# Kernel tuning notes

Hardware: AMD Instinct MI355X
Metric: run time of the kernel (lower is better)

## Reference

```python
import jax, jax.numpy as jnp
import numpy as np
from jax import lax

D = 256; NH = 8; LYR = 2; G = 64; K = G * G; T = 4; EC = 32
B = 4; N = 512; CITY = 256; DFF = 4 * D

def _conv(x, w):
    return lax.conv_general_dilated(x, w, (1, 1), 'SAME', dimension_numbers=('NCHW', 'OIHW', 'NCHW'))

def _ln(x, w, b):
    m = x.mean(-1, keepdims=True)
    v = ((x - m) ** 2).mean(-1, keepdims=True)
    return (x - m) / jnp.sqrt(v + 1e-5) * w + b

def _mlp(x, w1, b1, w2, b2):
    return jax.nn.gelu(x @ w1 + b1) @ w2 + b2

def setup_inputs():
    key = jax.random.key(0)
    ks = iter(jax.random.split(key, 64))
    def nrm(shape, s=0.02):
        return jax.random.normal(next(ks), shape, jnp.float32) * s
    return {
        'meas_xy': jax.random.uniform(next(ks), (B, N, 2), jnp.float32),
        'meas_v': jax.random.normal(next(ks), (B, N), jnp.float32),
        'bs_xy': jax.random.uniform(next(ks), (B, 1, 2), jnp.float32),
        'task_id': jax.random.randint(next(ks), (B,), 0, T),
        'city': jax.random.uniform(next(ks), (B, CITY, CITY), jnp.float32),
        'mp_w1': nrm((3, D)), 'mp_b1': jnp.zeros((D,)), 'mp_w2': nrm((D, D)), 'mp_b2': jnp.zeros((D,)),
        'bp_w1': nrm((2, D)), 'bp_b1': jnp.zeros((D,)), 'bp_w2': nrm((D, D)), 'bp_b2': jnp.zeros((D,)),
        'env_w1': nrm((EC, 1, 3, 3)), 'env_b1': jnp.zeros((EC,)),
        'env_w2': nrm((EC, EC, 3, 3)), 'env_b2': jnp.zeros((EC,)),
        'env_w3': nrm((D, EC, 1, 1)), 'env_b3': jnp.zeros((D,)),
        'task_emb': nrm((T, D)), 'tp_w': nrm((D, D)), 'tp_b': jnp.zeros((D,)),
        'grid_pos': nrm((K, D)),
        'blk_dens_w': nrm((LYR, D)), 'blk_dens_b': jnp.zeros((LYR, D)),
        'blk_ln1_w': jnp.ones((LYR, D)), 'blk_ln1_b': jnp.zeros((LYR, D)),
        'blk_wq': nrm((LYR, D, D)), 'blk_bq': jnp.zeros((LYR, D)),
        'blk_wk': nrm((LYR, D, D)), 'blk_bk': jnp.zeros((LYR, D)),
        'blk_wv': nrm((LYR, D, D)), 'blk_bv': jnp.zeros((LYR, D)),
        'blk_wo': nrm((LYR, D, D)), 'blk_bo': jnp.zeros((LYR, D)),
        'blk_ln2_w': jnp.ones((LYR, D)), 'blk_ln2_b': jnp.zeros((LYR, D)),
        'blk_ff_w1': nrm((LYR, D, DFF)), 'blk_ff_b1': jnp.zeros((LYR, DFF)),
        'blk_ff_w2': nrm((LYR, DFF, D)), 'blk_ff_b2': jnp.zeros((LYR, D)),
        'tfp_w': nrm((T, D, D)), 'tfp_b': jnp.zeros((T, D)),
        'head_w': nrm((D, 1)), 'head_b': jnp.zeros((1,)),
    }

def reference(meas_xy, meas_v, bs_xy, task_id, city, mp_w1, mp_b1, mp_w2, mp_b2, bp_w1, bp_b1, bp_w2, bp_b2, env_w1, env_b1, env_w2, env_b2, env_w3, env_b3, task_emb, tp_w, tp_b, grid_pos, blk_dens_w, blk_dens_b, blk_ln1_w, blk_ln1_b, blk_wq, blk_bq, blk_wk, blk_bk, blk_wv, blk_bv, blk_wo, blk_bo, blk_ln2_w, blk_ln2_b, blk_ff_w1, blk_ff_b1, blk_ff_w2, blk_ff_b2, tfp_w, tfp_b, head_w, head_b):
    b = meas_xy.shape[0]
    dh = D // NH
    # normalized grid cell centers, [K,2] in (x,y) order
    c = (jnp.arange(G, dtype=jnp.float32) + 0.5) / G
    gy, gx = jnp.meshgrid(c, c, indexing='ij')
    grid_xy = jnp.stack([gx, gy], -1).reshape(K, 2)
    meas_tok = _mlp(jnp.concatenate([meas_xy, meas_v[..., None]], -1), mp_w1, mp_b1, mp_w2, mp_b2)
    bs_tok = _mlp(bs_xy, bp_w1, bp_b1, bp_w2, bp_b2)
    src = jnp.concatenate([meas_tok, bs_tok], 1)       # [B,Ns,D]
    src_xy = jnp.concatenate([meas_xy, bs_xy], 1)      # [B,Ns,2]
    # distance bias: [B,K,Ns]
    attn_bias = -jnp.linalg.norm(grid_xy[None, :, None, :] - src_xy[:, None, :, :], axis=-1)
    # gaussian measurement density: [B,K]
    diff = grid_xy[None, :, None, :] - meas_xy[:, None, :, :]
    dist2 = (diff * diff).sum(-1)
    sigma = 0.08
    density = jnp.exp(-dist2 / (2.0 * sigma * sigma)).mean(-1)
    # env branch: nearest-resize city to GxG, small CNN
    idx = jnp.floor(jnp.arange(G) * (city.shape[1] / G)).astype(jnp.int32)
    city_grid = city[:, idx][:, :, idx][:, None]       # [B,1,G,G]
    h = jax.nn.gelu(_conv(city_grid, env_w1) + env_b1[None, :, None, None])
    h = jax.nn.gelu(_conv(h, env_w2) + env_b2[None, :, None, None])
    env_map = _conv(h, env_w3) + env_b3[None, :, None, None]
    env_grid = env_map.transpose(0, 2, 3, 1).reshape(b, K, D)
    task_vec = (task_emb[task_id] @ tp_w + tp_b)[:, None, :]
    grid = grid_pos[None] + task_vec + env_grid
    inv_sqrt = jnp.float32(1.0 / np.sqrt(dh))
    for l in range(LYR):
        # density modulation injected into the grid latent
        g = grid + density[..., None] * blk_dens_w[l] + blk_dens_b[l]
        hn = _ln(g, blk_ln1_w[l], blk_ln1_b[l])
        q = (hn @ blk_wq[l] + blk_bq[l]).reshape(b, K, NH, dh)
        kk = (src @ blk_wk[l] + blk_bk[l]).reshape(b, -1, NH, dh)
        vv = (src @ blk_wv[l] + blk_bv[l]).reshape(b, -1, NH, dh)
        scores = jnp.einsum('bkhd,bnhd->bhkn', q, kk) * inv_sqrt + attn_bias[:, None]
        a = jax.nn.softmax(scores, -1)
        o = jnp.einsum('bhkn,bnhd->bkhd', a, vv).reshape(b, K, D) @ blk_wo[l] + blk_bo[l]
        g = g + o
        g = g + _mlp(_ln(g, blk_ln2_w[l], blk_ln2_b[l]), blk_ff_w1[l], blk_ff_b1[l], blk_ff_w2[l], blk_ff_b2[l])
        grid = g
    # per-sample task projection from the weight bank
    tf = jax.nn.gelu(jnp.einsum('bkd,bdh->bkh', grid, tfp_w[task_id]) + tfp_b[task_id][:, None, :])
    logits = (tf @ head_w + head_b)[..., 0].reshape(b, G, G)
    return logits
```

## Files before the change

### kernel.cpp

```cpp
#include <hip/hip_runtime.h>
#include <hip/hip_bf16.h>
#include <math.h>

#define D 256
#define NH 8
#define DH 32
#define LYR 2
#define G 64
#define KK 4096
#define T 4
#define EC 32
#define B 4
#define N 512
#define CITY 256
#define DFF 1024
#define NS 513
#define NSP 544
#define MSRC 2052
#define MSRCP 2176
#define ISQ 0.17677669529663687f
#define LOG2E 1.4426950408889634f

typedef short bf16x8 __attribute__((ext_vector_type(8)));
typedef float f32x4 __attribute__((ext_vector_type(4)));

__device__ __forceinline__ float gelu_f(float x) {
    const float c2 = 2.f * 0.7978845608028654f * LOG2E;
    float u = x + 0.044715f * x * x * x;
    float e = __builtin_amdgcn_exp2f(-c2 * u);
    return x * __builtin_amdgcn_rcpf(1.f + e);
}

__device__ __forceinline__ unsigned short f2bf(float f) {
    unsigned int u = __float_as_uint(f);
    unsigned int r = (u + 0x7FFFu + ((u >> 16) & 1u)) >> 16;
    return (unsigned short)r;
}

__device__ __forceinline__ float bf2f(unsigned short u) {
    return __uint_as_float((unsigned)u << 16);
}

__device__ __forceinline__ unsigned cvtpk(float a, float b) {
    unsigned r;
    asm("v_cvt_pk_bf16_f32 %0, %1, %2" : "=v"(r) : "v"(a), "v"(b));
    return r;
}

__device__ __forceinline__ void gl2lds16(const unsigned short* g, unsigned short* l) {
    __builtin_amdgcn_global_load_lds(
        (const __attribute__((address_space(1))) unsigned int*)g,
        (__attribute__((address_space(3))) unsigned int*)l, 16, 0, 0);
}

__global__ __launch_bounds__(256) void pre1_k(
    const float* __restrict__ wq, const float* __restrict__ wk,
    const float* __restrict__ wv, const float* __restrict__ wo,
    const float* __restrict__ ff1, const float* __restrict__ ff2,
    const float* __restrict__ tfp,
    const float* __restrict__ bk, const float* __restrict__ bv,
    unsigned short* __restrict__ wqT, unsigned short* __restrict__ kvT,
    unsigned short* __restrict__ woT, unsigned short* __restrict__ ff1T,
    unsigned short* __restrict__ ff2T, unsigned short* __restrict__ tfpT,
    float* __restrict__ kvbias,
    const float* __restrict__ meas_xy, const float* __restrict__ meas_v,
    const float* __restrict__ bs_xy,
    const float* __restrict__ mp_w1, const float* __restrict__ mp_b1,
    const float* __restrict__ mp_w2, const float* __restrict__ mp_b2,
    const float* __restrict__ bp_w1, const float* __restrict__ bp_b1,
    const float* __restrict__ bp_w2, const float* __restrict__ bp_b2,
    unsigned short* __restrict__ srcbf, float* __restrict__ src_xy,
    float* __restrict__ dens,
    const float* __restrict__ city, const float* __restrict__ env_w1,
    const float* __restrict__ env_b1, float* __restrict__ h1,
    const float* __restrict__ task_emb, const int* __restrict__ task_id,
    const float* __restrict__ tp_w, const float* __restrict__ tp_b,
    float* __restrict__ tvec,
    unsigned short* __restrict__ khd, unsigned short* __restrict__ vch)
{
    __shared__ float sh[1088];
    int bx = blockIdx.x;
    int tid = threadIdx.x;
    if (bx < 1792) {
        const float* src; unsigned short* dst;
        int Kd, Nn, nmat, rowOff = 0, t; size_t matStride;
        if (bx < 512) {
            int job = bx >> 7; t = bx & 127;
            Kd = 256; Nn = 256; nmat = 2;
            if (job == 0)      { src = wq; dst = wqT; matStride = 65536; }
            else if (job == 1) { src = wk; dst = kvT; matStride = 131072; }
            else if (job == 2) { src = wv; dst = kvT; matStride = 131072; rowOff = 256; }
            else               { src = wo; dst = woT; matStride = 65536; }
            if ((t & 63) == 0 && job == 1) kvbias[(t >> 6) * 512 + tid] = bk[(t >> 6) * 256 + tid];
            if ((t & 63) == 0 && job == 2) kvbias[(t >> 6) * 512 + 256 + tid] = bv[(t >> 6) * 256 + tid];
        } else if (bx < 1024) { t = bx - 512;  src = ff1; dst = ff1T; Kd = 256;  Nn = 1024; nmat = 2; matStride = 262144; }
        else if (bx < 1536)   { t = bx - 1024; src = ff2; dst = ff2T; Kd = 1024; Nn = 256;  nmat = 2; matStride = 262144; }
        else                  { t = bx - 1536; src = tfp; dst = tfpT; Kd = 256;  Nn = 256;  nmat = 4; matStride = 65536; }
        int tn = Nn / 32, perMat = tn * (Kd / 32);
        int mat = t / perMat;
        int rem = t - mat * perMat;
        int nb = (rem % tn) * 32, kb = (rem / tn) * 32;
        const float* s = src + (size_t)mat * Kd * Nn;
        unsigned short* d = dst + (size_t)mat * matStride;
        float (*tb)[33] = (float (*)[33])sh;
        int tx = tid & 31, ty = tid >> 5;
        #pragma unroll
        for (int i = 0; i < 4; i++)
            tb[ty + i * 8][tx] = s[(size_t)(kb + ty + i * 8) * Nn + nb + tx];
        __syncthreads();
        #pragma unroll
        for (int i = 0; i < 4; i++)
            d[(size_t)(rowOff + nb + ty + i * 8) * Kd + kb + tx] = f2bf(tb[tx][ty + i * 8]);
    } else if (bx < 3968) {
        int id = bx - 1792;
        int dd = tid;
        if (id >= B * N + B) {
            srcbf[(size_t)id * D + dd] = 0;
            return;
        }
        float* hid = sh;
        int row;
        const float *w1, *b1, *w2, *b2;
        float x0, x1, x2 = 0.f;
        int nin;
        if (id < B * N) {
            int b = id >> 9, n = id & 511;
            x0 = meas_xy[(b * N + n) * 2 + 0];
            x1 = meas_xy[(b * N + n) * 2 + 1];
            x2 = meas_v[b * N + n];
            w1 = mp_w1; b1 = mp_b1; w2 = mp_w2; b2 = mp_b2; nin = 3;
            row = b * NS + n;
        } else {
            int b = id - B * N;
            x0 = bs_xy[b * 2 + 0];
            x1 = bs_xy[b * 2 + 1];
            w1 = bp_w1; b1 = bp_b1; w2 = bp_w2; b2 = bp_b2; nin = 2;
            row = b * NS + N;
        }
        float h = x0 * w1[dd] + x1 * w1[D + dd] + b1[dd];
        if (nin == 3) h += x2 * w1[2 * D + dd];
        hid[dd] = gelu_f(h);
        __syncthreads();
        float o = b2[dd];
        for (int j = 0; j < D; j++) o += hid[j] * w2[j * D + dd];
        srcbf[(size_t)row * D + dd] = f2bf(o);
        if (dd == 0) { src_xy[row * 2 + 0] = x0; src_xy[row * 2 + 1] = x1; }
    } else if (bx < 4032) {
        int blk = bx - 3968;
        int b = blk >> 4, kc = blk & 15;
        int k = kc * 256 + tid;
        float* mx = sh; float* my = sh + 512;
        for (int i = tid; i < N; i += 256) {
            mx[i] = meas_xy[(b * N + i) * 2 + 0];
            my[i] = meas_xy[(b * N + i) * 2 + 1];
        }
        __syncthreads();
        float gx = ((k & 63) + 0.5f) / 64.f;
        float gy = ((k >> 6) + 0.5f) / 64.f;
        float s = 0.f;
        for (int n = 0; n < N; n++) {
            float dx = gx - mx[n], dy = gy - my[n];
            s += __expf(-(dx * dx + dy * dy) * 78.125f);
        }
        dens[b * KK + k] = s * (1.f / (float)N);
    } else if (bx < 6080) {
        int i = (bx - 4032) * 256 + tid;
        int x = i & 63, y = (i >> 6) & 63, c = (i >> 12) & 31, b = i >> 17;
        float s = env_b1[c];
        for (int ky = 0; ky < 3; ky++) {
            int yy = y + ky - 1;
            if (yy < 0 || yy >= G) continue;
            for (int kx = 0; kx < 3; kx++) {
                int xx = x + kx - 1;
                if (xx < 0 || xx >= G) continue;
                s += city[(b * CITY + yy * 4) * CITY + xx * 4] * env_w1[c * 9 + ky * 3 + kx];
            }
        }
        h1[i] = gelu_f(s);
    } else if (bx < 6084) {
        int b = bx - 6080;
        float* e = sh;
        e[tid] = task_emb[task_id[b] * D + tid];
        __syncthreads();
        float s = tp_b[tid];
        for (int j = 0; j < D; j++) s += e[j] * tp_w[j * D + tid];
        tvec[b * D + tid] = s;
    } else {
        int bh = bx - 6084;
        unsigned short* kp = khd + ((size_t)bh * 544 + 513) * 32;
        for (int i = tid; i < 992; i += 256) kp[i] = 0;
        unsigned short* vp = vch + ((size_t)bh * 17 + 16) * 1024;
        for (int i = tid; i < 1024; i += 256) vp[i] = 0;
    }
}

__global__ __launch_bounds__(256) void conv2_k(
    const float* __restrict__ h1, const float* __restrict__ w,
    const float* __restrict__ bias, float* __restrict__ h2) {
    int blk = blockIdx.x;
    int yt = blk & 15, cg = (blk >> 4) & 7, b = blk >> 7;
    int x = threadIdx.x & 63, y = yt * 4 + (threadIdx.x >> 6);
    int c0 = cg * 4;
    float flag[9];
    int off[9];
    #pragma unroll
    for (int ky = 0; ky < 3; ky++) {
        int yy = y + ky - 1;
        bool vy = (yy >= 0 && yy < G);
        int yc = min(max(yy, 0), G - 1);
        #pragma unroll
        for (int kx = 0; kx < 3; kx++) {
            int xx = x + kx - 1;
            bool vx = (xx >= 0 && xx < G);
            int xc = min(max(xx, 0), G - 1);
            flag[ky * 3 + kx] = (vy && vx) ? 1.f : 0.f;
            off[ky * 3 + kx] = yc * G + xc;
        }
    }
    const float* hp = h1 + ((size_t)(b * EC) << 12);
    float acc[4] = {bias[c0], bias[c0 + 1], bias[c0 + 2], bias[c0 + 3]};
    float v[9], nv[9];
    #pragma unroll
    for (int t = 0; t < 9; t++) v[t] = hp[off[t]] * flag[t];
    for (int ci = 0; ci < EC; ci++) {
        if (ci < EC - 1) {
            const float* hn = hp + ((size_t)(ci + 1) << 12);
            #pragma unroll
            for (int t = 0; t < 9; t++) nv[t] = hn[off[t]] * flag[t];
        }
        #pragma unroll
        for (int cc = 0; cc < 4; cc++) {
            const float* wp = w + ((size_t)(c0 + cc) * EC + ci) * 9;
            #pragma unroll
            for (int t = 0; t < 9; t++) acc[cc] += v[t] * wp[t];
        }
        #pragma unroll
        for (int t = 0; t < 9; t++) v[t] = nv[t];
    }
    size_t obase = (((size_t)(b * EC + c0)) << 12) + y * G + x;
    #pragma unroll
    for (int cc = 0; cc < 4; cc++)
        h2[obase + ((size_t)cc << 12)] = gelu_f(acc[cc]);
}

__global__ __launch_bounds__(256) void pre2_k(
    const float* __restrict__ h2, const float* __restrict__ w3,
    const float* __restrict__ b3, const float* __restrict__ grid_pos,
    const float* __restrict__ tvec, float* __restrict__ grid,
    float* __restrict__ out, const float* __restrict__ head_b)
{
    __shared__ float sh[1088];
    int bx = blockIdx.x;
    int tid = threadIdx.x;
    if (bx < 2048) {
        int b = bx >> 9, k0 = (bx & 511) * 8;
        float (*h2s)[8] = (float (*)[8])sh;
        h2s[tid >> 3][tid & 7] = h2[(((size_t)b * EC + (tid >> 3)) << 12) + k0 + (tid & 7)];
        float w3r[32];
        #pragma unroll
        for (int c4 = 0; c4 < 8; c4++) {
            float4 w4 = *(const float4*)(w3 + tid * 32 + c4 * 4);
            w3r[c4 * 4 + 0] = w4.x; w3r[c4 * 4 + 1] = w4.y;
            w3r[c4 * 4 + 2] = w4.z; w3r[c4 * 4 + 3] = w4.w;
        }
        float base = b3[tid] + tvec[b * D + tid];
        __syncthreads();
        #pragma unroll
        for (int j = 0; j < 8; j++) {
            float s = base + grid_pos[(size_t)(k0 + j) * D + tid];
            #pragma unroll
            for (int ci = 0; ci < 32; ci++) s += h2s[ci][j] * w3r[ci];
            grid[((size_t)b * KK + k0 + j) * D + tid] = s;
        }
    } else {
        out[(bx - 2048) * 256 + tid] = head_b[0];
    }
}

template <int DENS>
__global__ __launch_bounds__(256) void dens_ln_k(
    float* __restrict__ grid, const float* __restrict__ dens,
    const float* __restrict__ dw, const float* __restrict__ db,
    const float* __restrict__ lw, const float* __restrict__ lb,
    unsigned short* __restrict__ y) {
    int row = blockIdx.x * 4 + (threadIdx.x >> 6);
    int lane = threadIdx.x & 63;
    float* gp = grid + (size_t)row * D + lane * 4;
    float4 v = *(float4*)gp;
    if (DENS) {
        float de = dens[row];
        float4 w4 = *(const float4*)(dw + lane * 4);
        float4 b4 = *(const float4*)(db + lane * 4);
        v.x += de * w4.x + b4.x; v.y += de * w4.y + b4.y;
        v.z += de * w4.z + b4.z; v.w += de * w4.w + b4.w;
        *(float4*)gp = v;
    }
    float s = v.x + v.y + v.z + v.w;
    #pragma unroll
    for (int o = 32; o > 0; o >>= 1) s += __shfl_xor(s, o);
    float mean = s * (1.f / D);
    float cx = v.x - mean, cy = v.y - mean, cz = v.z - mean, cw = v.w - mean;
    float q = cx * cx + cy * cy + cz * cz + cw * cw;
    #pragma unroll
    for (int o = 32; o > 0; o >>= 1) q += __shfl_xor(q, o);
    float inv = rsqrtf(q * (1.f / D) + 1e-5f);
    float4 lwv = *(const float4*)(lw + lane * 4);
    float4 lbv = *(const float4*)(lb + lane * 4);
    ushort4 o4;
    o4.x = f2bf(cx * inv * lwv.x + lbv.x);
    o4.y = f2bf(cy * inv * lwv.y + lbv.y);
    o4.z = f2bf(cz * inv * lwv.z + lbv.z);
    o4.w = f2bf(cw * inv * lwv.w + lbv.w);
    *(ushort4*)(y + (size_t)row * D + lane * 4) = o4;
}

template <int GELU, int ACCUM, int OBF, int TFPH, int STBF, int KVT = 0>
__device__ __forceinline__ void gemm_core(
    const unsigned short* __restrict__ A, const unsigned short* __restrict__ Wt,
    const float* __restrict__ bias, void* __restrict__ Cv,
    int M, int K, int Nn, int bn, int bm,
    const float* __restrict__ hw, unsigned short* __restrict__ Xb, float scale,
    unsigned short* As, unsigned short* Bs) {
    int tid = threadIdx.x;
    int wave = tid >> 6, lane = tid & 63;
    int q4 = lane >> 4, lr = lane & 15;
    int wn = wave * 16;
    int srow = tid >> 2;
    int sk8 = ((tid & 3) ^ ((tid >> 3) & 3)) * 8;
    const unsigned short* Ap  = A  + (size_t)(bm + srow) * K + sk8;
    const unsigned short* Bp0 = Wt + (size_t)(bn + srow) * K + sk8;
    unsigned short* AsD = As + tid * 8;
    unsigned short* BsD = Bs + tid * 8;
    int q4x = (q4 ^ ((lr >> 1) & 3)) * 8;
    f32x4 acc[4] = {};

    gl2lds16(Ap,       AsD);
    gl2lds16(Ap + 32,  AsD + 2048);
    gl2lds16(Bp0,      BsD);
    gl2lds16(Bp0 + 32, BsD + 2048);

    int nk = K >> 6;
    for (int ki = 0; ki < nk; ki++) {
        __syncthreads();
        if (ki + 1 < nk) {
            int k0 = (ki + 1) << 6;
            int nb = ((ki + 1) & 1) * 4096;
            gl2lds16(Ap + k0,       AsD + nb);
            gl2lds16(Ap + k0 + 32,  AsD + nb + 2048);
            gl2lds16(Bp0 + k0,      BsD + nb);
            gl2lds16(Bp0 + k0 + 32, BsD + nb + 2048);
        }
        int cb = (ki & 1) * 4096;
        #pragma unroll
        for (int ks = 0; ks < 2; ks++) {
            bf16x8 af[4], bf;
            #pragma unroll
            for (int i = 0; i < 4; i++)
                af[i] = *(const bf16x8*)&As[cb + ks * 2048 + (i * 16 + lr) * 32 + q4x];
            bf = *(const bf16x8*)&Bs[cb + ks * 2048 + (wn + lr) * 32 + q4x];
            #pragma unroll
            for (int i = 0; i < 4; i++)
                acc[i] = __builtin_amdgcn_mfma_f32_16x16x32_bf16(af[i], bf, acc[i], 0, 0, 0);
        }
    }

    if (KVT) {
        int gc = bn + wn + lr;
        float bv = bias[gc];
        bool isV = gc >= 256;
        #pragma unroll
        for (int i = 0; i < 4; i++) {
            #pragma unroll
            for (int r = 0; r < 4; r++) {
                int gr = bm + i * 16 + q4 * 4 + r;
                if (gr < MSRC) {
                    float v = acc[i][r] + bv;
                    int bb = gr / NS;
                    int tok = gr - bb * NS;
                    if (!isV) {
                        int h = gc >> 5, dh = gc & 31;
                        int t32 = tok & 31;
                        int kkp = ((t32 & 1) << 4) | ((t32 >> 3) << 2) | ((t32 >> 1) & 3);
                        int tokP = (tok & ~31) | kkp;
                        ((unsigned short*)Cv)[(((size_t)(bb * 8 + h) * 544) + tokP) * 32 + dh] = f2bf(v);
                    } else {
                        int gcv = gc - 256;
                        int h = gcv >> 5, dh = gcv & 31;
                        int c = tok >> 5, t32 = tok & 31;
                        Xb[((((size_t)(bb * 8 + h) * 17 + c) * 32 + dh)) * 32 + t32] = f2bf(v);
                    }
                }
            }
        }
        return;
    }

    int gc = bn + wn + lr;
    float bv = bias[gc];
    #pragma unroll
    for (int i = 0; i < 4; i++) {
        #pragma unroll
        for (int r = 0; r < 4; r++) {
            int gr = bm + i * 16 + q4 * 4 + r;
            if (gr < M) {
                float v = (acc[i][r] + bv) * scale;
                if (GELU) v = gelu_f(v);
                size_t idx = (size_t)gr * Nn + gc;
                if (OBF) {
                    ((unsigned short*)Cv)[idx] = f2bf(v);
                } else if (ACCUM) {
                    float nv = ((float*)Cv)[idx] + v;
                    ((float*)Cv)[idx] = nv;
                    if (STBF) Xb[idx] = f2bf(nv);
                } else {
                    ((float*)Cv)[idx] = v;
                }
            }
        }
    }
}

template <int GELU, int ACCUM, int OBF, int STBF>
__device__ __forceinline__ void gemm128_core(
    const unsigned short* __restrict__ A, const unsigned short* __restrict__ Wt,
    const float* __restrict__ bias, void* __restrict__ Cv,
    int K, int Nn, int bn, int bm, float scale, unsigned short* __restrict__ Xb,
    unsigned short* As, unsigned short* Bs) {
    int tid = threadIdx.x;
    int wave = tid >> 6, lane = tid & 63;
    int q4 = lane >> 4, lr = lane & 15;
    int wn = wave * 16;
    int srow = tid >> 2;
    int sk8 = ((tid & 3) ^ ((tid >> 3) & 3)) * 8;
    const unsigned short* Ap  = A + (size_t)(bm + srow) * K + sk8;
    const unsigned short* Ap2 = Ap + (size_t)64 * K;
    const unsigned short* Bp  = Wt + (size_t)(bn + srow) * K + sk8;
    unsigned short* AsD = As + tid * 8;
    unsigned short* BsD = Bs + tid * 8;
    int q4x = (q4 ^ ((lr >> 1) & 3)) * 8;
    f32x4 acc[8] = {};

    gl2lds16(Ap,        AsD);
    gl2lds16(Ap2,       AsD + 2048);
    gl2lds16(Ap + 32,   AsD + 4096);
    gl2lds16(Ap2 + 32,  AsD + 6144);
    gl2lds16(Bp,        BsD);
    gl2lds16(Bp + 32,   BsD + 2048);

    int nk = K >> 6;
    for (int ki = 0; ki < nk; ki++) {
        __syncthreads();
        if (ki + 1 < nk) {
            int k0 = (ki + 1) << 6;
            int nbA = ((ki + 1) & 1) * 8192;
            int nbB = ((ki + 1) & 1) * 4096;
            gl2lds16(Ap + k0,        AsD + nbA);
            gl2lds16(Ap2 + k0,       AsD + nbA + 2048);
            gl2lds16(Ap + k0 + 32,   AsD + nbA + 4096);
            gl2lds16(Ap2 + k0 + 32,  AsD + nbA + 6144);
            gl2lds16(Bp + k0,        BsD + nbB);
            gl2lds16(Bp + k0 + 32,   BsD + nbB + 2048);
        }
        int cbA = (ki & 1) * 8192, cbB = (ki & 1) * 4096;
        #pragma unroll
        for (int ks = 0; ks < 2; ks++) {
            bf16x8 bf = *(const bf16x8*)&Bs[cbB + ks * 2048 + (wn + lr) * 32 + q4x];
            #pragma unroll
            for (int i = 0; i < 8; i++) {
                bf16x8 af = *(const bf16x8*)&As[cbA + ks * 4096 + (i * 16 + lr) * 32 + q4x];
                acc[i] = __builtin_amdgcn_mfma_f32_16x16x32_bf16(af, bf, acc[i], 0, 0, 0);
            }
        }
    }

    int gc = bn + wn + lr;
    float bv = bias[gc];
    #pragma unroll
    for (int i = 0; i < 8; i++) {
        #pragma unroll
        for (int r = 0; r < 4; r++) {
            int gr = bm + i * 16 + q4 * 4 + r;
            float v = (acc[i][r] + bv) * scale;
            if (GELU) v = gelu_f(v);
            size_t idx = (size_t)gr * Nn + gc;
            if (OBF) {
                ((unsigned short*)Cv)[idx] = f2bf(v);
            } else if (ACCUM) {
                float nv = ((float*)Cv)[idx] + v;
                ((float*)Cv)[idx] = nv;
                if (STBF) Xb[idx] = f2bf(nv);
            } else {
                ((float*)Cv)[idx] = v;
            }
        }
    }
}

template <int GELU, int ACCUM, int OBF, int STBF>
__global__ __launch_bounds__(256) void gemm128_k(
    const unsigned short* __restrict__ A, const unsigned short* __restrict__ Wt,
    const float* __restrict__ bias, void* __restrict__ Cv,
    int M, int K, int Nn, int nx, float scale, unsigned short* __restrict__ Xb) {
    __shared__ unsigned short As[16384];
    __shared__ unsigned short Bs[8192];
    int nwg = gridDim.x;
    int bid = blockIdx.x;
    int wgid = (bid & 7) * (nwg >> 3) + (bid >> 3);
    int bn = (wgid % nx) * 64;
    int bm = (wgid / nx) * 128;
    gemm128_core<GELU, ACCUM, OBF, STBF>(A, Wt, bias, Cv, K, Nn, bn, bm, scale, Xb, As, Bs);
}

__global__ __launch_bounds__(256) void qkv128_k(
    const unsigned short* __restrict__ xbf, const unsigned short* __restrict__ wqT,
    const float* __restrict__ bq, unsigned short* __restrict__ qbf,
    const unsigned short* __restrict__ srcbf, const unsigned short* __restrict__ kvT,
    const float* __restrict__ kvb, unsigned short* __restrict__ khd,
    unsigned short* __restrict__ vch) {
    __shared__ unsigned short As[16384];
    __shared__ unsigned short Bs[8192];
    int bid = blockIdx.x;
    if (bid < 512) {
        int wgid = (bid & 7) * 64 + (bid >> 3);
        int bn = (wgid & 3) * 64;
        int bm = (wgid >> 2) * 128;
        gemm128_core<0, 0, 1, 0>(xbf, wqT, bq, qbf, D, D, bn, bm,
                                 ISQ * LOG2E, nullptr, As, Bs);
    } else {
        int idx = bid - 512;
        gemm_core<0, 0, 1, 0, 0, 1>(srcbf, kvT, kvb, khd, MSRC, D, 512,
                                    (idx & 7) * 64, (idx >> 3) * 64, nullptr, vch, 1.f, As, Bs);
    }
}

__global__ __launch_bounds__(256) void tfp128_k(
    const unsigned short* __restrict__ A, const unsigned short* __restrict__ Wt0,
    const float* __restrict__ bias0, float* __restrict__ Cv,
    const int* __restrict__ task_id, const float* __restrict__ hw) {
    __shared__ unsigned short As[16384];
    __shared__ unsigned short Bs[8192];
    int nwg = gridDim.x;
    int bid = blockIdx.x;
    int wgid = (bid & 7) * (nwg >> 3) + (bid >> 3);
    int bn = (wgid & 3) * 64;
    int bm = (wgid >> 2) * 128;
    int tid = threadIdx.x;
    int wave = tid >> 6, lane = tid & 63;
    int q4 = lane >> 4, lr = lane & 15;
    int wn = wave * 16;
    int t = task_id[bm >> 12];
    const unsigned short* Wt = Wt0 + (size_t)t * D * D;
    const float* bias = bias0 + t * D;
    int srow = tid >> 2;
    int sk8 = ((tid & 3) ^ ((tid >> 3) & 3)) * 8;
    const unsigned short* Ap  = A + (size_t)(bm + srow) * D + sk8;
    const unsigned short* Ap2 = Ap + (size_t)64 * D;
    const unsigned short* Bp  = Wt + (size_t)(bn + srow) * D + sk8;
    unsigned short* AsD = As + tid * 8;
    unsigned short* BsD = Bs + tid * 8;
    int q4x = (q4 ^ ((lr >> 1) & 3)) * 8;
    f32x4 acc[8] = {};

    gl2lds16(Ap,        AsD);
    gl2lds16(Ap2,       AsD + 2048);
    gl2lds16(Ap + 32,   AsD + 4096);
    gl2lds16(Ap2 + 32,  AsD + 6144);
    gl2lds16(Bp,        BsD);
    gl2lds16(Bp + 32,   BsD + 2048);

    int nk = D >> 6;
    for (int ki = 0; ki < nk; ki++) {
        __syncthreads();
        if (ki + 1 < nk) {
            int k0 = (ki + 1) << 6;
            int nbA = ((ki + 1) & 1) * 8192;
            int nbB = ((ki + 1) & 1) * 4096;
            gl2lds16(Ap + k0,        AsD + nbA);
            gl2lds16(Ap2 + k0,       AsD + nbA + 2048);
            gl2lds16(Ap + k0 + 32,   AsD + nbA + 4096);
            gl2lds16(Ap2 + k0 + 32,  AsD + nbA + 6144);
            gl2lds16(Bp + k0,        BsD + nbB);
            gl2lds16(Bp + k0 + 32,   BsD + nbB + 2048);
        }
        int cbA = (ki & 1) * 8192, cbB = (ki & 1) * 4096;
        #pragma unroll
        for (int ks = 0; ks < 2; ks++) {
            bf16x8 bf = *(const bf16x8*)&Bs[cbB + ks * 2048 + (wn + lr) * 32 + q4x];
            #pragma unroll
            for (int i = 0; i < 8; i++) {
                bf16x8 af = *(const bf16x8*)&As[cbA + ks * 4096 + (i * 16 + lr) * 32 + q4x];
                acc[i] = __builtin_amdgcn_mfma_f32_16x16x32_bf16(af, bf, acc[i], 0, 0, 0);
            }
        }
    }

    int gc = bn + wn + lr;
    float bv = bias[gc];
    float hv = hw[gc];
    #pragma unroll
    for (int i = 0; i < 8; i++) {
        #pragma unroll
        for (int r = 0; r < 4; r++) {
            float s = gelu_f(acc[i][r] + bv) * hv;
            s += __shfl_xor(s, 1); s += __shfl_xor(s, 2);
            s += __shfl_xor(s, 4); s += __shfl_xor(s, 8);
            if (lr == 0)
                atomicAdd(Cv + (bm + i * 16 + q4 * 4 + r), s);
        }
    }
}

__global__ __launch_bounds__(256) void attn_mfma(
    const unsigned short* __restrict__ qb,
    const unsigned short* __restrict__ khd,
    const unsigned short* __restrict__ vch,
    const float* __restrict__ sxy,
    unsigned short* __restrict__ out)
{
    __shared__ float2 sxys[NSP];
    int bid = blockIdx.x;
    int qp = bid & 31, h = (bid >> 5) & 7, b = bid >> 8;
    int qt0 = qp * 2;
    int tid = threadIdx.x, wave = tid >> 6, lane = tid & 63;
    int q4 = lane >> 4, lr = lane & 15;

    int cell0 = qt0 * 64 + wave * 16 + lr;
    size_t qrow0 = (size_t)(b * KK + cell0);
    size_t qrow1 = qrow0 + 64;
    bf16x8 qfA = *(const bf16x8*)(qb + qrow0 * D + h * DH + q4 * 8);
    bf16x8 qfB = *(const bf16x8*)(qb + qrow1 * D + h * DH + q4 * 8);
    const unsigned short* kp0 = khd + ((size_t)(b * 8 + h) * 544) * 32 + lr * 32 + q4 * 8;
    const unsigned short* vb0 = vch + ((size_t)(b * 8 + h) * 17) * 1024 + lr * 32 + q4 * 8;

    float lla0 = 0.f, lla1 = 0.f, llb0 = 0.f, llb1 = 0.f;
    f32x4 o0a = {0.f, 0.f, 0.f, 0.f}, o1a = {0.f, 0.f, 0.f, 0.f};
    f32x4 o0b = {0.f, 0.f, 0.f, 0.f}, o1b = {0.f, 0.f, 0.f, 0.f};

    bf16x8 k0X, k1X, v0X, v1X, k0Y, k1Y, v0Y, v1Y;
    f32x4 d0X, d1X, d0Y, d1Y;
    f32x4 e0X, e1X, e0Y, e1Y;

#define LDK(S, c) { size_t co = (size_t)(c) * 1024; \
    k0##S = *(const bf16x8*)(kp0 + co); k1##S = *(const bf16x8*)(kp0 + co + 512); }
#define LDV(S, c) { size_t co = (size_t)(c) * 1024; \
    v0##S = *(const bf16x8*)(vb0 + co); v1##S = *(const bf16x8*)(vb0 + co + 512); }

    LDK(X, 0); LDV(X, 0);
    LDK(Y, 1); LDV(Y, 1);

    const float2* sb = (const float2*)(sxy + 2 * (size_t)b * NS);
    for (int i = tid; i < NSP; i += 256) {
        float2 v = (i < NS) ? sb[i] : make_float2(1.e4f, 1.e4f);
        sxys[i] = make_float2(v.x * LOG2E, v.y * LOG2E);
    }
    __syncthreads();

    int qi = wave * 16 + lr;
    float gxp  = (qi + 0.5f) * (1.f / 64.f) * LOG2E;
    float gy0p = (qt0 + 0.5f) * (1.f / 64.f) * LOG2E;
    float gy1p = (qt0 + 1.5f) * (1.f / 64.f) * LOG2E;
    const float2* spf = &sxys[q4 * 8];

#define DIST2(xx, yy, dq0, dq1) { float dx_ = gxp - (xx); float dx2_ = dx_ * dx_; \
    float dy0_ = gy0p - (yy); dq0 = __builtin_amdgcn_sqrtf(__builtin_fmaf(dy0_, dy0_, dx2_)); \
    float dy1_ = gy1p - (yy); dq1 = __builtin_amdgcn_sqrtf(__builtin_fmaf(dy1_, dy1_, dx2_)); }
#define LDB(S, c) { const float4* p4_ = (const float4*)(spf + (size_t)(c) * 32); \
    float4 a0_ = p4_[0], a1_ = p4_[1], a2_ = p4_[2], a3_ = p4_[3]; \
    DIST2(a0_.x, a0_.y, d0##S[0], e0##S[0]); DIST2(a0_.z, a0_.w, d1##S[0], e1##S[0]); \
    DIST2(a1_.x, a1_.y, d0##S[1], e0##S[1]); DIST2(a1_.z, a1_.w, d1##S[1], e1##S[1]); \
    DIST2(a2_.x, a2_.y, d0##S[2], e0##S[2]); DIST2(a2_.z, a2_.w, d1##S[2], e1##S[2]); \
    DIST2(a3_.x, a3_.y, d0##S[3], e0##S[3]); DIST2(a3_.z, a3_.w, d1##S[3], e1##S[3]); }

    LDB(X, 0); LDB(Y, 1);

#define BODY(S, cp) { \
    f32x4 s0a = {0.f, 0.f, 0.f, 0.f}, s1a = {0.f, 0.f, 0.f, 0.f}; \
    f32x4 s0b = {0.f, 0.f, 0.f, 0.f}, s1b = {0.f, 0.f, 0.f, 0.f}; \
    s0a = __builtin_amdgcn_mfma_f32_16x16x32_bf16(k0##S, qfA, s0a, 0, 0, 0); \
    s1a = __builtin_amdgcn_mfma_f32_16x16x32_bf16(k1##S, qfA, s1a, 0, 0, 0); \
    s0b = __builtin_amdgcn_mfma_f32_16x16x32_bf16(k0##S, qfB, s0b, 0, 0, 0); \
    s1b = __builtin_amdgcn_mfma_f32_16x16x32_bf16(k1##S, qfB, s1b, 0, 0, 0); \
    LDK(S, cp); \
    float p0a[4], p1a[4], p0b[4], p1b[4]; \
    p0a[0] = __builtin_amdgcn_exp2f(s0a[0] - d0##S[0]); \
    p0a[1] = __builtin_amdgcn_exp2f(s0a[1] - d0##S[1]); \
    p0a[2] = __builtin_amdgcn_exp2f(s0a[2] - d0##S[2]); \
    p0a[3] = __builtin_amdgcn_exp2f(s0a[3] - d0##S[3]); \
    p1a[0] = __builtin_amdgcn_exp2f(s1a[0] - d1##S[0]); \
    p1a[1] = __builtin_amdgcn_exp2f(s1a[1] - d1##S[1]); \
    p1a[2] = __builtin_amdgcn_exp2f(s1a[2] - d1##S[2]); \
    p1a[3] = __builtin_amdgcn_exp2f(s1a[3] - d1##S[3]); \
    p0b[0] = __builtin_amdgcn_exp2f(s0b[0] - e0##S[0]); \
    p0b[1] = __builtin_amdgcn_exp2f(s0b[1] - e0##S[1]); \
    p0b[2] = __builtin_amdgcn_exp2f(s0b[2] - e0##S[2]); \
    p0b[3] = __builtin_amdgcn_exp2f(s0b[3] - e0##S[3]); \
    p1b[0] = __builtin_amdgcn_exp2f(s1b[0] - e1##S[0]); \
    p1b[1] = __builtin_amdgcn_exp2f(s1b[1] - e1##S[1]); \
    p1b[2] = __builtin_amdgcn_exp2f(s1b[2] - e1##S[2]); \
    p1b[3] = __builtin_amdgcn_exp2f(s1b[3] - e1##S[3]); \
    LDB(S, cp); \
    lla0 += (p0a[0] + p0a[1]) + (p0a[2] + p0a[3]); \
    lla1 += (p1a[0] + p1a[1]) + (p1a[2] + p1a[3]); \
    llb0 += (p0b[0] + p0b[1]) + (p0b[2] + p0b[3]); \
    llb1 += (p1b[0] + p1b[1]) + (p1b[2] + p1b[3]); \
    union { unsigned u[4]; bf16x8 v; } pua, pub; \
    pua.u[0] = cvtpk(p0a[0], p1a[0]); \
    pua.u[1] = cvtpk(p0a[1], p1a[1]); \
    pua.u[2] = cvtpk(p0a[2], p1a[2]); \
    pua.u[3] = cvtpk(p0a[3], p1a[3]); \
    pub.u[0] = cvtpk(p0b[0], p1b[0]); \
    pub.u[1] = cvtpk(p0b[1], p1b[1]); \
    pub.u[2] = cvtpk(p0b[2], p1b[2]); \
    pub.u[3] = cvtpk(p0b[3], p1b[3]); \
    o0a = __builtin_amdgcn_mfma_f32_16x16x32_bf16(v0##S, pua.v, o0a, 0, 0, 0); \
    o1a = __builtin_amdgcn_mfma_f32_16x16x32_bf16(v1##S, pua.v, o1a, 0, 0, 0); \
    o0b = __builtin_amdgcn_mfma_f32_16x16x32_bf16(v0##S, pub.v, o0b, 0, 0, 0); \
    o1b = __builtin_amdgcn_mfma_f32_16x16x32_bf16(v1##S, pub.v, o1b, 0, 0, 0); \
    LDV(S, cp); \
}

    for (int c = 0; c < 16; c += 2) {
        int cpX = c + 2;
        int cpY = (c + 3 > 16) ? 16 : c + 3;
        BODY(X, cpX);
        BODY(Y, cpY);
    }
    BODY(X, 16);

#undef BODY
#undef LDB
#undef DIST2
#undef LDK
#undef LDV

    float lla = lla0 + lla1;
    lla += __shfl_xor(lla, 16);
    lla += __shfl_xor(lla, 32);
    float inva = 1.f / lla;
    float llb = llb0 + llb1;
    llb += __shfl_xor(llb, 16);
    llb += __shfl_xor(llb, 32);
    float invb = 1.f / llb;
    uint2 sa0, sa1, sb0, sb1;
    sa0.x = cvtpk(o0a[0] * inva, o0a[1] * inva);
    sa0.y = cvtpk(o0a[2] * inva, o0a[3] * inva);
    sa1.x = cvtpk(o1a[0] * inva, o1a[1] * inva);
    sa1.y = cvtpk(o1a[2] * inva, o1a[3] * inva);
    sb0.x = cvtpk(o0b[0] * invb, o0b[1] * invb);
    sb0.y = cvtpk(o0b[2] * invb, o0b[3] * invb);
    sb1.x = cvtpk(o1b[0] * invb, o1b[1] * invb);
    sb1.y = cvtpk(o1b[2] * invb, o1b[3] * invb);
    *(uint2*)(out + qrow0 * D + h * DH + q4 * 4) = sa0;
    *(uint2*)(out + qrow0 * D + h * DH + 16 + q4 * 4) = sa1;
    *(uint2*)(out + qrow1 * D + h * DH + q4 * 4) = sb0;
    *(uint2*)(out + qrow1 * D + h * DH + 16 + q4 * 4) = sb1;
}

extern "C" void kernel_launch(void* const* d_in, const int* in_sizes, int n_in,
                              void* d_out, int out_size, void* d_ws, size_t ws_size,
                              hipStream_t stream) {
    const float* meas_xy = (const float*)d_in[0];
    const float* meas_v  = (const float*)d_in[1];
    const float* bs_xy   = (const float*)d_in[2];
    const int*   task_id = (const int*)d_in[3];
    const float* city    = (const float*)d_in[4];
    const float* mp_w1 = (const float*)d_in[5];  const float* mp_b1 = (const float*)d_in[6];
    const float* mp_w2 = (const float*)d_in[7];  const float* mp_b2 = (const float*)d_in[8];
    const float* bp_w1 = (const float*)d_in[9];  const float* bp_b1 = (const float*)d_in[10];
    const float* bp_w2 = (const float*)d_in[11]; const float* bp_b2 = (const float*)d_in[12];
    const float* env_w1 = (const float*)d_in[13]; const float* env_b1 = (const float*)d_in[14];
    const float* env_w2 = (const float*)d_in[15]; const float* env_b2 = (const float*)d_in[16];
    const float* env_w3 = (const float*)d_in[17]; const float* env_b3 = (const float*)d_in[18];
    const float* task_emb = (const float*)d_in[19];
    const float* tp_w = (const float*)d_in[20]; const float* tp_b = (const float*)d_in[21];
    const float* grid_pos = (const float*)d_in[22];
    const float* dens_w = (const float*)d_in[23]; const float* dens_b = (const float*)d_in[24];
    const float* ln1_w = (const float*)d_in[25]; const float* ln1_b = (const float*)d_in[26];
    const float* wq = (const float*)d_in[27]; const float* bq = (const float*)d_in[28];
    const float* wk = (const float*)d_in[29]; const float* bk = (const float*)d_in[30];
    const float* wv = (const float*)d_in[31]; const float* bv = (const float*)d_in[32];
    const float* wo = (const float*)d_in[33]; const float* bo = (const float*)d_in[34];
    const float* ln2_w = (const float*)d_in[35]; const float* ln2_b = (const float*)d_in[36];
    const float* ff_w1 = (const float*)d_in[37]; const float* ff_b1 = (const float*)d_in[38];
    const float* ff_w2 = (const float*)d_in[39]; const float* ff_b2 = (const float*)d_in[40];
    const float* tfp_w = (const float*)d_in[41]; const float* tfp_b = (const float*)d_in[42];
    const float* head_w = (const float*)d_in[43]; const float* head_b = (const float*)d_in[44];
    float* out = (float*)d_out;

    float* ws = (float*)d_ws;
    size_t off = 0;
    float* src_xy = ws + off; off += (size_t)B * NS * 2 + 128;
    float* dens   = ws + off; off += (size_t)B * KK;
    float* tvec   = ws + off; off += (size_t)B * D;
    float* h1     = ws + off; off += (size_t)B * EC * KK;
    float* grid   = ws + off; off += (size_t)B * KK * D;
    unsigned short* srcbf = (unsigned short*)(ws + off); off += (size_t)MSRCP * D / 2;
    unsigned short* khd   = (unsigned short*)(ws + off); off += (size_t)B * 8 * 544 * 32 / 2;
    unsigned short* vch   = (unsigned short*)(ws + off); off += (size_t)B * 8 * 17 * 1024 / 2;
    float* qreg   = ws + off; off += (size_t)B * KK * D / 2;
    unsigned short* qbf = (unsigned short*)qreg;
    float* h2     = qreg;
    unsigned short* xbf    = (unsigned short*)(ws + off); off += (size_t)B * KK * D / 2;
    unsigned short* attnbf = (unsigned short*)(ws + off); off += (size_t)B * KK * D / 2;
    unsigned short* hidbf  = (unsigned short*)(ws + off); off += (size_t)B * KK * DFF / 2;
    unsigned short* wqT  = (unsigned short*)(ws + off); off += (size_t)LYR * D * D / 2;
    unsigned short* kvT  = (unsigned short*)(ws + off); off += (size_t)LYR * 512 * D / 2;
    unsigned short* woT  = (unsigned short*)(ws + off); off += (size_t)LYR * D * D / 2;
    unsigned short* ff1T = (unsigned short*)(ws + off); off += (size_t)LYR * D * DFF / 2;
    unsigned short* ff2T = (unsigned short*)(ws + off); off += (size_t)LYR * DFF * D / 2;
    unsigned short* tfpT = (unsigned short*)(ws + off); off += (size_t)T * D * D / 2;
    float* kvbias = ws + off; off += (size_t)LYR * 512;
    (void)ws_size; (void)n_in; (void)in_sizes; (void)out_size;

    const int M = B * KK;

    pre1_k<<<6116, 256, 0, stream>>>(
        wq, wk, wv, wo, ff_w1, ff_w2, tfp_w, bk, bv,
        wqT, kvT, woT, ff1T, ff2T, tfpT, kvbias,
        meas_xy, meas_v, bs_xy, mp_w1, mp_b1, mp_w2, mp_b2,
        bp_w1, bp_b1, bp_w2, bp_b2, srcbf, src_xy,
        dens, city, env_w1, env_b1, h1,
        task_emb, task_id, tp_w, tp_b, tvec, khd, vch);
    conv2_k<<<512, 256, 0, stream>>>(h1, env_w2, env_b2, h2);
    pre2_k<<<2112, 256, 0, stream>>>(h2, env_w3, env_b3, grid_pos, tvec, grid,
                                     out, head_b);

    for (int l = 0; l < LYR; l++) {
        dens_ln_k<1><<<M / 4, 256, 0, stream>>>(grid, dens, dens_w + l * D, dens_b + l * D,
                                                ln1_w + l * D, ln1_b + l * D, xbf);
        qkv128_k<<<784, 256, 0, stream>>>(
            xbf, wqT + (size_t)l * D * D, bq + l * D, qbf,
            srcbf, kvT + (size_t)l * 512 * D, kvbias + l * 512, khd, vch);
        attn_mfma<<<B * NH * 32, 256, 0, stream>>>(qbf, khd, vch, src_xy, attnbf);
        gemm128_k<0, 1, 0, 0><<<512, 256, 0, stream>>>(
            attnbf, woT + (size_t)l * D * D, bo + l * D, grid, M, D, D, 4, 1.f, nullptr);
        dens_ln_k<0><<<M / 4, 256, 0, stream>>>(grid, nullptr, nullptr, nullptr,
                                                ln2_w + l * D, ln2_b + l * D, xbf);
        gemm128_k<1, 0, 1, 0><<<2048, 256, 0, stream>>>(
            xbf, ff1T + (size_t)l * D * DFF, ff_b1 + l * DFF, hidbf, M, D, DFF, 16, 1.f, nullptr);
        if (l == 0) {
            gemm128_k<0, 1, 0, 0><<<512, 256, 0, stream>>>(
                hidbf, ff2T + (size_t)l * DFF * D, ff_b2 + l * D, grid, M, DFF, D, 4, 1.f, nullptr);
        } else {
            gemm128_k<0, 1, 0, 1><<<512, 256, 0, stream>>>(
                hidbf, ff2T + (size_t)l * DFF * D, ff_b2 + l * D, grid, M, DFF, D, 4, 1.f, xbf);
        }
    }
    tfp128_k<<<512, 256, 0, stream>>>(xbf, tfpT, tfp_b, out, task_id, head_w);
}
```

Before: 479.9 us.

## Process four query rows per attention block to reuse K/V tiles

Each attention block now handles four 64-cell query rows instead of two, halving the grid to 512 blocks. Every K/V chunk and source-coordinate tile loaded per block is reused across twice as many queries, cutting global and LDS traffic. The x-distance term is precomputed per chunk and the full distance bias is now computed inline per row. The cost is higher register pressure from eight output accumulators, and fewer blocks, which lowers occupancy and parallelism on a GPU with many CUs.

```diff
diff --git a/kernel.cpp b/kernel.cpp
--- a/kernel.cpp
+++ b/kernel.cpp
@@ -619,26 +619,29 @@
 {
     __shared__ float2 sxys[NSP];
     int bid = blockIdx.x;
-    int qp = bid & 31, h = (bid >> 5) & 7, b = bid >> 8;
-    int qt0 = qp * 2;
+    int qq = bid & 15, h = (bid >> 4) & 7, b = bid >> 7;
+    int qt0 = qq * 4;
     int tid = threadIdx.x, wave = tid >> 6, lane = tid & 63;
     int q4 = lane >> 4, lr = lane & 15;
 
     int cell0 = qt0 * 64 + wave * 16 + lr;
     size_t qrow0 = (size_t)(b * KK + cell0);
-    size_t qrow1 = qrow0 + 64;
-    bf16x8 qfA = *(const bf16x8*)(qb + qrow0 * D + h * DH + q4 * 8);
-    bf16x8 qfB = *(const bf16x8*)(qb + qrow1 * D + h * DH + q4 * 8);
+    bf16x8 qfa = *(const bf16x8*)(qb + qrow0 * D + h * DH + q4 * 8);
+    bf16x8 qfb = *(const bf16x8*)(qb + (qrow0 + 64) * D + h * DH + q4 * 8);
+    bf16x8 qfc = *(const bf16x8*)(qb + (qrow0 + 128) * D + h * DH + q4 * 8);
+    bf16x8 qfd = *(const bf16x8*)(qb + (qrow0 + 192) * D + h * DH + q4 * 8);
     const unsigned short* kp0 = khd + ((size_t)(b * 8 + h) * 544) * 32 + lr * 32 + q4 * 8;
     const unsigned short* vb0 = vch + ((size_t)(b * 8 + h) * 17) * 1024 + lr * 32 + q4 * 8;
 
-    float lla0 = 0.f, lla1 = 0.f, llb0 = 0.f, llb1 = 0.f;
-    f32x4 o0a = {0.f, 0.f, 0.f, 0.f}, o1a = {0.f, 0.f, 0.f, 0.f};
-    f32x4 o0b = {0.f, 0.f, 0.f, 0.f}, o1b = {0.f, 0.f, 0.f, 0.f};
+    float lla = 0.f, llb = 0.f, llc = 0.f, lld = 0.f;
+    f32x4 o0a = {0.f,0.f,0.f,0.f}, o1a = {0.f,0.f,0.f,0.f};
+    f32x4 o0b = {0.f,0.f,0.f,0.f}, o1b = {0.f,0.f,0.f,0.f};
+    f32x4 o0c = {0.f,0.f,0.f,0.f}, o1c = {0.f,0.f,0.f,0.f};
+    f32x4 o0d = {0.f,0.f,0.f,0.f}, o1d = {0.f,0.f,0.f,0.f};
 
     bf16x8 k0X, k1X, v0X, v1X, k0Y, k1Y, v0Y, v1Y;
-    f32x4 d0X, d1X, d0Y, d1Y;
-    f32x4 e0X, e1X, e0Y, e1Y;
+    f32x4 x20X, x21X, ey0X, ey1X;
+    f32x4 x20Y, x21Y, ey0Y, ey1Y;
 
 #define LDK(S, c) { size_t co = (size_t)(c) * 1024; \
     k0##S = *(const bf16x8*)(kp0 + co); k1##S = *(const bf16x8*)(kp0 + co + 512); }
@@ -659,101 +662,93 @@
     float gxp  = (qi + 0.5f) * (1.f / 64.f) * LOG2E;
     float gy0p = (qt0 + 0.5f) * (1.f / 64.f) * LOG2E;
     float gy1p = (qt0 + 1.5f) * (1.f / 64.f) * LOG2E;
+    float gy2p = (qt0 + 2.5f) * (1.f / 64.f) * LOG2E;
+    float gy3p = (qt0 + 3.5f) * (1.f / 64.f) * LOG2E;
     const float2* spf = &sxys[q4 * 8];
 
-#define DIST2(xx, yy, dq0, dq1) { float dx_ = gxp - (xx); float dx2_ = dx_ * dx_; \
-    float dy0_ = gy0p - (yy); dq0 = __builtin_amdgcn_sqrtf(__builtin_fmaf(dy0_, dy0_, dx2_)); \
-    float dy1_ = gy1p - (yy); dq1 = __builtin_amdgcn_sqrtf(__builtin_fmaf(dy1_, dy1_, dx2_)); }
 #define LDB(S, c) { const float4* p4_ = (const float4*)(spf + (size_t)(c) * 32); \
     float4 a0_ = p4_[0], a1_ = p4_[1], a2_ = p4_[2], a3_ = p4_[3]; \
-    DIST2(a0_.x, a0_.y, d0##S[0], e0##S[0]); DIST2(a0_.z, a0_.w, d1##S[0], e1##S[0]); \
-    DIST2(a1_.x, a1_.y, d0##S[1], e0##S[1]); DIST2(a1_.z, a1_.w, d1##S[1], e1##S[1]); \
-    DIST2(a2_.x, a2_.y, d0##S[2], e0##S[2]); DIST2(a2_.z, a2_.w, d1##S[2], e1##S[2]); \
-    DIST2(a3_.x, a3_.y, d0##S[3], e0##S[3]); DIST2(a3_.z, a3_.w, d1##S[3], e1##S[3]); }
+    float ex_; \
+    ex_ = gxp - a0_.x; x20##S[0] = ex_ * ex_; ey0##S[0] = a0_.y; \
+    ex_ = gxp - a0_.z; x21##S[0] = ex_ * ex_; ey1##S[0] = a0_.w; \
+    ex_ = gxp - a1_.x; x20##S[1] = ex_ * ex_; ey0##S[1] = a1_.y; \
+    ex_ = gxp - a1_.z; x21##S[1] = ex_ * ex_; ey1##S[1] = a1_.w; \
+    ex_ = gxp - a2_.x; x20##S[2] = ex_ * ex_; ey0##S[2] = a2_.y; \
+    ex_ = gxp - a2_.z; x21##S[2] = ex_ * ex_; ey1##S[2] = a2_.w; \
+    ex_ = gxp - a3_.x; x20##S[3] = ex_ * ex_; ey0##S[3] = a3_.y; \
+    ex_ = gxp - a3_.z; x21##S[3] = ex_ * ex_; ey1##S[3] = a3_.w; }
 
     LDB(X, 0); LDB(Y, 1);
 
+#define DEXP(s_, x2_, ey_, gyr) ({ float dy_ = (gyr) - (ey_); \
+    __builtin_amdgcn_exp2f((s_) - __builtin_amdgcn_sqrtf(__builtin_fmaf(dy_, dy_, (x2_)))); })
+
+#define ROW(S, r, gyr) { \
+    f32x4 s0_ = {0.f,0.f,0.f,0.f}, s1_ = {0.f,0.f,0.f,0.f}; \
+    s0_ = __builtin_amdgcn_mfma_f32_16x16x32_bf16(k0##S, qf##r, s0_, 0, 0, 0); \
+    s1_ = __builtin_amdgcn_mfma_f32_16x16x32_bf16(k1##S, qf##r, s1_, 0, 0, 0); \
+    float p0_[4], p1_[4]; \
+    p0_[0] = DEXP(s0_[0], x20##S[0], ey0##S[0], gyr); \
+    p0_[1] = DEXP(s0_[1], x20##S[1], ey0##S[1], gyr); \
+    p0_[2] = DEXP(s0_[2], x20##S[2], ey0##S[2], gyr); \
+    p0_[3] = DEXP(s0_[3], x20##S[3], ey0##S[3], gyr); \
+    p1_[0] = DEXP(s1_[0], x21##S[0], ey1##S[0], gyr); \
+    p1_[1] = DEXP(s1_[1], x21##S[1], ey1##S[1], gyr); \
+    p1_[2] = DEXP(s1_[2], x21##S[2], ey1##S[2], gyr); \
+    p1_[3] = DEXP(s1_[3], x21##S[3], ey1##S[3], gyr); \
+    ll##r += ((p0_[0] + p0_[1]) + (p0_[2] + p0_[3])) + ((p1_[0] + p1_[1]) + (p1_[2] + p1_[3])); \
+    union { unsigned u[4]; bf16x8 v; } pu_; \
+    pu_.u[0] = cvtpk(p0_[0], p1_[0]); \
+    pu_.u[1] = cvtpk(p0_[1], p1_[1]); \
+    pu_.u[2] = cvtpk(p0_[2], p1_[2]); \
+    pu_.u[3] = cvtpk(p0_[3], p1_[3]); \
+    o0##r = __builtin_amdgcn_mfma_f32_16x16x32_bf16(v0##S, pu_.v, o0##r, 0, 0, 0); \
+    o1##r = __builtin_amdgcn_mfma_f32_16x16x32_bf16(v1##S, pu_.v, o1##r, 0, 0, 0); \
+}
+
 #define BODY(S, cp) { \
-    f32x4 s0a = {0.f, 0.f, 0.f, 0.f}, s1a = {0.f, 0.f, 0.f, 0.f}; \
-    f32x4 s0b = {0.f, 0.f, 0.f, 0.f}, s1b = {0.f, 0.f, 0.f, 0.f}; \
-    s0a = __builtin_amdgcn_mfma_f32_16x16x32_bf16(k0##S, qfA, s0a, 0, 0, 0); \
-    s1a = __builtin_amdgcn_mfma_f32_16x16x32_bf16(k1##S, qfA, s1a, 0, 0, 0); \
-    s0b = __builtin_amdgcn_mfma_f32_16x16x32_bf16(k0##S, qfB, s0b, 0, 0, 0); \
-    s1b = __builtin_amdgcn_mfma_f32_16x16x32_bf16(k1##S, qfB, s1b, 0, 0, 0); \
+    ROW(S, a, gy0p); \
+    ROW(S, b, gy1p); \
+    ROW(S, c, gy2p); \
+    ROW(S, d, gy3p); \
     LDK(S, cp); \
-    float p0a[4], p1a[4], p0b[4], p1b[4]; \
-    p0a[0] = __builtin_amdgcn_exp2f(s0a[0] - d0##S[0]); \
-    p0a[1] = __builtin_amdgcn_exp2f(s0a[1] - d0##S[1]); \
-    p0a[2] = __builtin_amdgcn_exp2f(s0a[2] - d0##S[2]); \
-    p0a[3] = __builtin_amdgcn_exp2f(s0a[3] - d0##S[3]); \
-    p1a[0] = __builtin_amdgcn_exp2f(s1a[0] - d1##S[0]); \
-    p1a[1] = __builtin_amdgcn_exp2f(s1a[1] - d1##S[1]); \
-    p1a[2] = __builtin_amdgcn_exp2f(s1a[2] - d1##S[2]); \
-    p1a[3] = __builtin_amdgcn_exp2f(s1a[3] - d1##S[3]); \
-    p0b[0] = __builtin_amdgcn_exp2f(s0b[0] - e0##S[0]); \
-    p0b[1] = __builtin_amdgcn_exp2f(s0b[1] - e0##S[1]); \
-    p0b[2] = __builtin_amdgcn_exp2f(s0b[2] - e0##S[2]); \
-    p0b[3] = __builtin_amdgcn_exp2f(s0b[3] - e0##S[3]); \
-    p1b[0] = __builtin_amdgcn_exp2f(s1b[0] - e1##S[0]); \
-    p1b[1] = __builtin_amdgcn_exp2f(s1b[1] - e1##S[1]); \
-    p1b[2] = __builtin_amdgcn_exp2f(s1b[2] - e1##S[2]); \
-    p1b[3] = __builtin_amdgcn_exp2f(s1b[3] - e1##S[3]); \
     LDB(S, cp); \
-    lla0 += (p0a[0] + p0a[1]) + (p0a[2] + p0a[3]); \
-    lla1 += (p1a[0] + p1a[1]) + (p1a[2] + p1a[3]); \
-    llb0 += (p0b[0] + p0b[1]) + (p0b[2] + p0b[3]); \
-    llb1 += (p1b[0] + p1b[1]) + (p1b[2] + p1b[3]); \
-    union { unsigned u[4]; bf16x8 v; } pua, pub; \
-    pua.u[0] = cvtpk(p0a[0], p1a[0]); \
-    pua.u[1] = cvtpk(p0a[1], p1a[1]); \
-    pua.u[2] = cvtpk(p0a[2], p1a[2]); \
-    pua.u[3] = cvtpk(p0a[3], p1a[3]); \
-    pub.u[0] = cvtpk(p0b[0], p1b[0]); \
-    pub.u[1] = cvtpk(p0b[1], p1b[1]); \
-    pub.u[2] = cvtpk(p0b[2], p1b[2]); \
-    pub.u[3] = cvtpk(p0b[3], p1b[3]); \
-    o0a = __builtin_amdgcn_mfma_f32_16x16x32_bf16(v0##S, pua.v, o0a, 0, 0, 0); \
-    o1a = __builtin_amdgcn_mfma_f32_16x16x32_bf16(v1##S, pua.v, o1a, 0, 0, 0); \
-    o0b = __builtin_amdgcn_mfma_f32_16x16x32_bf16(v0##S, pub.v, o0b, 0, 0, 0); \
-    o1b = __builtin_amdgcn_mfma_f32_16x16x32_bf16(v1##S, pub.v, o1b, 0, 0, 0); \
     LDV(S, cp); \
 }
 
-    for (int c = 0; c < 16; c += 2) {
-        int cpX = c + 2;
-        int cpY = (c + 3 > 16) ? 16 : c + 3;
+    for (int cc = 0; cc < 16; cc += 2) {
+        int cpX = cc + 2;
+        int cpY = (cc + 3 > 16) ? 16 : cc + 3;
         BODY(X, cpX);
         BODY(Y, cpY);
     }
     BODY(X, 16);
 
 #undef BODY
+#undef ROW
+#undef DEXP
 #undef LDB
-#undef DIST2
 #undef LDK
 #undef LDV
 
-    float lla = lla0 + lla1;
-    lla += __shfl_xor(lla, 16);
-    lla += __shfl_xor(lla, 32);
-    float inva = 1.f / lla;
-    float llb = llb0 + llb1;
-    llb += __shfl_xor(llb, 16);
-    llb += __shfl_xor(llb, 32);
-    float invb = 1.f / llb;
-    uint2 sa0, sa1, sb0, sb1;
-    sa0.x = cvtpk(o0a[0] * inva, o0a[1] * inva);
-    sa0.y = cvtpk(o0a[2] * inva, o0a[3] * inva);
-    sa1.x = cvtpk(o1a[0] * inva, o1a[1] * inva);
-    sa1.y = cvtpk(o1a[2] * inva, o1a[3] * inva);
-    sb0.x = cvtpk(o0b[0] * invb, o0b[1] * invb);
-    sb0.y = cvtpk(o0b[2] * invb, o0b[3] * invb);
-    sb1.x = cvtpk(o1b[0] * invb, o1b[1] * invb);
-    sb1.y = cvtpk(o1b[2] * invb, o1b[3] * invb);
-    *(uint2*)(out + qrow0 * D + h * DH + q4 * 4) = sa0;
-    *(uint2*)(out + qrow0 * D + h * DH + 16 + q4 * 4) = sa1;
-    *(uint2*)(out + qrow1 * D + h * DH + q4 * 4) = sb0;
-    *(uint2*)(out + qrow1 * D + h * DH + 16 + q4 * 4) = sb1;
+#define FINROW(r, rowoff) { \
+    float ll_ = ll##r; \
+    ll_ += __shfl_xor(ll_, 16); \
+    ll_ += __shfl_xor(ll_, 32); \
+    float inv_ = 1.f / ll_; \
+    uint2 s0_, s1_; \
+    s0_.x = cvtpk(o0##r[0] * inv_, o0##r[1] * inv_); \
+    s0_.y = cvtpk(o0##r[2] * inv_, o0##r[3] * inv_); \
+    s1_.x = cvtpk(o1##r[0] * inv_, o1##r[1] * inv_); \
+    s1_.y = cvtpk(o1##r[2] * inv_, o1##r[3] * inv_); \
+    *(uint2*)(out + (qrow0 + (rowoff)) * D + h * DH + q4 * 4) = s0_; \
+    *(uint2*)(out + (qrow0 + (rowoff)) * D + h * DH + 16 + q4 * 4) = s1_; \
+}
+    FINROW(a, 0);
+    FINROW(b, 64);
+    FINROW(c, 128);
+    FINROW(d, 192);
+#undef FINROW
 }
 
 extern "C" void kernel_launch(void* const* d_in, const int* in_sizes, int n_in,
@@ -831,7 +826,7 @@
         qkv128_k<<<784, 256, 0, stream>>>(
             xbf, wqT + (size_t)l * D * D, bq + l * D, qbf,
             srcbf, kvT + (size_t)l * 512 * D, kvbias + l * 512, khd, vch);
-        attn_mfma<<<B * NH * 32, 256, 0, stream>>>(qbf, khd, vch, src_xy, attnbf);
+        attn_mfma<<<B * NH * 16, 256, 0, stream>>>(qbf, khd, vch, src_xy, attnbf);
         gemm128_k<0, 1, 0, 0><<<512, 256, 0, stream>>>(
             attnbf, woT + (size_t)l * D * D, bo + l * D, grid, M, D, D, 4, 1.f, nullptr);
         dens_ln_k<0><<<M / 4, 256, 0, stream>>>(grid, nullptr, nullptr, nullptr,
```

After: 477.6 us (median of 2 runs). Within noise of the previous version (-0.5%).
